# Kernel tuning notes

Measured on AMD Instinct MI355X. Metric: run time of the kernel, lower is better.

The kernel has to match this reference:

```python
import jax, jax.numpy as jnp
import numpy as np

B, N, D = 8, 4096, 256
MLP_DIM = int(2.0 * D * 2)  # mlp_expansion_factor * dim * 2


def setup_inputs() -> dict:
    key = jax.random.key(0)
    ks = jax.random.split(key, 16)
    s = 0.02  # small init for MLP linears (torch Linear default is small-uniform)
    return {
        'h':  jax.random.normal(ks[0], (B, N, D), jnp.float32),
        'x1': jax.random.normal(ks[1], (B, N, D, 3), jnp.float32),  # degree 1, m=3
        'x2': jax.random.normal(ks[2], (B, N, D, 5), jnp.float32),  # degree 2, m=5
        # per-degree projections (torch.randn init, unscaled, per source)
        'proj1': jax.random.normal(ks[3], (D, D), jnp.float32),
        'proj2': jax.random.normal(ks[4], (D, D), jnp.float32),
        'pre1':  jax.random.normal(ks[5], (D, D), jnp.float32),
        'pre2':  jax.random.normal(ks[6], (D, D), jnp.float32),
        # per-degree 2-layer MLPs: Linear(2D, MLP_DIM) -> SiLU -> Linear(MLP_DIM, 2D)
        'w1_0': jax.random.normal(ks[7], (2 * D, MLP_DIM), jnp.float32) * s,
        'b1_0': jnp.zeros((MLP_DIM,), jnp.float32),
        'w2_0': jax.random.normal(ks[8], (MLP_DIM, 2 * D), jnp.float32) * s,
        'b2_0': jnp.zeros((2 * D,), jnp.float32),
        'w1_1': jax.random.normal(ks[9], (2 * D, MLP_DIM), jnp.float32) * s,
        'b1_1': jnp.zeros((MLP_DIM,), jnp.float32),
        'w2_1': jax.random.normal(ks[10], (MLP_DIM, 2 * D), jnp.float32) * s,
        'b2_1': jnp.zeros((2 * D,), jnp.float32),
    }


def _one_degree(h, x, pre, proj, w1, b1, w2, b2):
    # x: (b, n, d, m); project channels for the invariant branch
    pm = jnp.einsum('bndm,de->bnem', x, pre)            # (b, n, d, m)
    inv = jnp.sqrt(jnp.sum(pm * pm, axis=-1))           # L2 norm over m -> (b, n, d)
    mlp_in = jnp.concatenate([h, inv], axis=-1)         # (b, n, 2d)
    hid = jax.nn.silu(mlp_in @ w1 + b1)                 # (b, n, mlp_dim)
    out = hid @ w2 + b2                                 # (b, n, 2d)
    m1, m2 = out[..., :D], out[..., D:]                 # each (b, n, d)
    p = jnp.einsum('bndm,de->bnem', x, proj)            # (b, n, d, m)
    mod = p * m2[..., None]                             # per-channel gating over m
    return m1, mod


def reference(h, x1, x2, proj1, proj2, pre1, pre2,
              w1_0, b1_0, w2_0, b2_0, w1_1, b1_1, w2_1, b2_1):
    m1_a, mod1 = _one_degree(h, x1, pre1, proj1, w1_0, b1_0, w2_0, b2_0)
    m1_b, mod2 = _one_degree(h, x2, pre2, proj2, w1_1, b1_1, w2_1, b2_1)
    h_new = h + m1_a + m1_b
    return (h_new, x1 + mod1, x2 + mod2)
```

## Files before the change

kernel.cpp:

```cpp
#include <hip/hip_runtime.h>
#include <hip/hip_bf16.h>

#define BN    32768
#define DD    256
#define MLPD  1024
#define TWOD  512

typedef __attribute__((ext_vector_type(8))) short short8;
typedef __attribute__((ext_vector_type(4))) float f32x4;

using bf16 = __hip_bfloat16;

__device__ __forceinline__ float bf2f(bf16 v){ return __bfloat162float(v); }
__device__ __forceinline__ bf16  f2bf(float v){ return __float2bfloat16(v); }

__device__ __forceinline__ void gl_lds16(const bf16* g, bf16* l) {
    __builtin_amdgcn_global_load_lds(
        (const __attribute__((address_space(1))) void*)(g),
        (__attribute__((address_space(3))) void*)(l),
        16, 0, 0);
}

__global__ void kprep(const float* __restrict__ pre1, const float* __restrict__ pre2,
                      const float* __restrict__ proj1, const float* __restrict__ proj2,
                      const float* __restrict__ w10, const float* __restrict__ w11,
                      const float* __restrict__ w20, const float* __restrict__ w21,
                      const float* __restrict__ h,
                      bf16* __restrict__ preT, bf16* __restrict__ projT,
                      bf16* __restrict__ w1T, bf16* __restrict__ w2T,
                      bf16* __restrict__ hbf)
{
    const long T0 = 131072, T1 = 131072, T2 = 1048576, T3 = 1048576, T4 = 8388608;
    const long total = T0 + T1 + T2 + T3 + T4;
    for (long i = (long)blockIdx.x * blockDim.x + threadIdx.x; i < total;
         i += (long)gridDim.x * blockDim.x) {
        long t = i;
        if (t < T0) {
            int d = (int)(t >> 16); int r = (int)(t & 65535); int e = r >> 8, k = r & 255;
            preT[t] = f2bf((d ? pre2 : pre1)[k*256 + e]);
        } else if ((t -= T0) < T1) {
            int d = (int)(t >> 16); int r = (int)(t & 65535); int e = r >> 8, k = r & 255;
            projT[t] = f2bf((d ? proj2 : proj1)[k*256 + e]);
        } else if ((t -= T1) < T2) {
            int d = (int)(t >> 19); int r = (int)(t & 524287); int j = r >> 9, k = r & 511;
            w1T[t] = f2bf((d ? w11 : w10)[k*1024 + j]);
        } else if ((t -= T2) < T3) {
            int d = (int)(t >> 19); int r = (int)(t & 524287); int n = r >> 10, k = r & 1023;
            w2T[t] = f2bf((d ? w21 : w20)[k*512 + n]);
        } else {
            t -= T3;
            hbf[t] = f2bf(h[t]);
        }
    }
}

template<int M, int ST>
__global__ __launch_bounds__(256) void kxT(const float* __restrict__ x,
                                           char* __restrict__ outb)
{
    __shared__ float raw[8*256*M];
    const int tid = threadIdx.x;
    const long tok0 = (long)blockIdx.x * 8;
    const float4* src = (const float4*)(x + tok0*256*M);
    const int n4 = (8*256*M)/4;
    for (int i = tid; i < n4; i += 256)
        ((float4*)raw)[i] = src[i];
    __syncthreads();
    const int nOut = 8*M*32;
    for (int i = tid; i < nOut; i += 256) {
        int d8 = i & 31;
        int tm = i >> 5;
        int t = tm / M, m = tm - t*M;
        short8 v;
#pragma unroll
        for (int j = 0; j < 8; j++) {
            bf16 bv = f2bf(raw[(t*256 + d8*8 + j)*M + m]);
            v[j] = *reinterpret_cast<short*>(&bv);
        }
        *(short8*)(outb + (size_t)(tok0 + t)*ST + m*512 + d8*16) = v;
    }
}

template<int M, int ST, bool MOD>
__global__ __launch_bounds__(256) void kxg(const char* __restrict__ xtb,
                                           const bf16* __restrict__ Bmat,
                                           bf16* __restrict__ invp,
                                           const bf16* __restrict__ m2p,
                                           const float* __restrict__ x,
                                           float* __restrict__ xout)
{
    __shared__ bf16 As[M*512];
    __shared__ bf16 Bs[8192];
    const int tid = threadIdx.x;
    const int lane = tid & 63, w = tid >> 6;
    const int lh = lane >> 4, l15 = lane & 15;
    const long tok0 = (long)blockIdx.x * 16;

    f32x4 acc[M][4];
#pragma unroll
    for (int m = 0; m < M; m++)
#pragma unroll
        for (int c = 0; c < 4; c++) acc[m][c] = (f32x4){0.f,0.f,0.f,0.f};

    for (int kc = 0; kc < 8; kc++) {
        for (int m = w; m < M; m += 4) {
            const char* src = xtb + (size_t)(tok0 + (lane >> 2))*ST
                              + m*512 + kc*64 + (lane & 3)*16;
            gl_lds16((const bf16*)src, As + m*512);
        }
#pragma unroll
        for (int i = 0; i < 4; i++) {
            int row = i*64 + (tid >> 2);
            gl_lds16(Bmat + row*256 + kc*32 + (tid & 3)*8, Bs + i*2048 + w*512);
        }
        __syncthreads();
        short8 a[M], b[4];
#pragma unroll
        for (int m = 0; m < M; m++)
            a[m] = *(const short8*)&As[m*512 + l15*32 + lh*8];
#pragma unroll
        for (int ct = 0; ct < 4; ct++)
            b[ct] = *(const short8*)&Bs[(w*64 + ct*16 + l15)*32 + lh*8];
#pragma unroll
        for (int m = 0; m < M; m++)
#pragma unroll
            for (int ct = 0; ct < 4; ct++)
                acc[m][ct] = __builtin_amdgcn_mfma_f32_16x16x32_bf16(a[m], b[ct], acc[m][ct], 0, 0, 0);
        __syncthreads();
    }

    if constexpr (!MOD) {
#pragma unroll
        for (int ct = 0; ct < 4; ct++) {
#pragma unroll
            for (int i = 0; i < 4; i++) {
                long t = tok0 + lh*4 + i;
                int e = w*64 + ct*16 + l15;
                float s = 0.f;
#pragma unroll
                for (int m = 0; m < M; m++) { float p = acc[m][ct][i]; s += p*p; }
                invp[t*256 + e] = f2bf(sqrtf(s));
            }
        }
    } else {
#pragma unroll
        for (int ct = 0; ct < 4; ct++) {
#pragma unroll
            for (int i = 0; i < 4; i++) {
                long t = tok0 + lh*4 + i;
                int e = w*64 + ct*16 + l15;
                float m2v = bf2f(m2p[t*256 + e]);
#pragma unroll
                for (int m = 0; m < M; m++) {
                    long gi = (t*256 + e)*(long)M + m;
                    xout[gi] = x[gi] + acc[m][ct][i]*m2v;
                }
            }
        }
    }
}

__global__ __launch_bounds__(512) void kmlp1(const bf16* __restrict__ hbf,
                                             const bf16* __restrict__ invws,
                                             const bf16* __restrict__ w1T,
                                             const float* __restrict__ b1_0,
                                             const float* __restrict__ b1_1,
                                             char* __restrict__ x1b,
                                             char* __restrict__ x2b,
                                             bf16* __restrict__ hid1b)
{
    __shared__ bf16 As[128*32];
    __shared__ bf16 Bs[256*32];
    const int tid = threadIdx.x;
    const int lane = tid & 63, w = tid >> 6;
    const int wr = w >> 2, wc = w & 3;
    const int lh = lane >> 4, l15 = lane & 15;

    const int bid   = ((blockIdx.x & 7) << 8) | (blockIdx.x >> 3);
    const int d     = bid >> 10;
    const int r     = bid & 1023;
    const int mtile = r >> 2;
    const int ntile = r & 3;
    const long tok0 = (long)mtile * 128;
    const int  j0   = ntile * 256;

    const bf16* Ahb = hbf   + (size_t)tok0 * 256;
    const bf16* Ain = invws + (size_t)d * BN * 256 + (size_t)tok0 * 256;
    const bf16* Bw  = w1T   + (size_t)d * MLPD * TWOD;
    const float* b1 = d ? b1_1 : b1_0;

    const int srow = tid >> 2;
    const int scol = (tid & 3) * 8;

    f32x4 acc[4][4];
#pragma unroll
    for (int ai = 0; ai < 4; ai++)
#pragma unroll
        for (int bj = 0; bj < 4; bj++) acc[ai][bj] = (f32x4){0.f,0.f,0.f,0.f};

    for (int kc = 0; kc < 16; kc++) {
        {
            const bf16* src = (kc < 8)
                ? Ahb + (size_t)srow*256 + kc*32 + scol
                : Ain + (size_t)srow*256 + (kc - 8)*32 + scol;
            gl_lds16(src, As + w*512);
        }
#pragma unroll
        for (int i = 0; i < 2; i++) {
            gl_lds16(Bw + (size_t)(j0 + i*128 + srow)*512 + kc*32 + scol,
                     Bs + i*4096 + w*512);
        }
        __syncthreads();
        short8 a[4], b[4];
#pragma unroll
        for (int ai = 0; ai < 4; ai++)
            a[ai] = *(const short8*)&As[(wr*64 + ai*16 + l15)*32 + lh*8];
#pragma unroll
        for (int bj = 0; bj < 4; bj++)
            b[bj] = *(const short8*)&Bs[(wc*64 + bj*16 + l15)*32 + lh*8];
#pragma unroll
        for (int ai = 0; ai < 4; ai++)
#pragma unroll
            for (int bj = 0; bj < 4; bj++)
                acc[ai][bj] = __builtin_amdgcn_mfma_f32_16x16x32_bf16(a[ai], b[bj], acc[ai][bj], 0, 0, 0);
        __syncthreads();
    }

#pragma unroll
    for (int ai = 0; ai < 4; ai++) {
#pragma unroll
        for (int bj = 0; bj < 4; bj++) {
#pragma unroll
            for (int i = 0; i < 4; i++) {
                long t = tok0 + wr*64 + ai*16 + lh*4 + i;
                int  j = j0 + wc*64 + bj*16 + l15;
                float v = acc[ai][bj][i] + b1[j];
                float s = v / (1.0f + __expf(-v));
                bf16 sb = f2bf(s);
                if (d == 0) {
                    *(bf16*)(x2b + (size_t)t*5120 + 2560 + j*2) = sb;
                } else {
                    if (j < 768) *(bf16*)(x1b + (size_t)t*3072 + 1536 + j*2) = sb;
                    else         hid1b[t*256 + (j - 768)] = sb;
                }
            }
        }
    }
}

__global__ __launch_bounds__(512) void kmlp2(const char* __restrict__ x1b,
                                             const char* __restrict__ x2b,
                                             const bf16* __restrict__ hid1b,
                                             const bf16* __restrict__ w2T,
                                             const float* __restrict__ b2_0,
                                             const float* __restrict__ b2_1,
                                             const float* __restrict__ h,
                                             bf16* __restrict__ m2ws,
                                             float* __restrict__ hout)
{
    __shared__ bf16 As[128*32];
    __shared__ bf16 Bs[256*32];
    const int tid = threadIdx.x;
    const int lane = tid & 63, w = tid >> 6;
    const int wr = w >> 2, wc = w & 3;
    const int lh = lane >> 4, l15 = lane & 15;

    const int bid   = (blockIdx.x & 7)*96 + (blockIdx.x >> 3);
    const int mtile = bid / 3;
    const int slot  = bid - mtile*3;
    const long tok0 = (long)mtile * 128;
    const bool is_m1 = (slot == 0);
    const int n0  = is_m1 ? 0 : 256;
    const int dm2 = is_m1 ? 0 : (slot - 1);
    const int nIter = is_m1 ? 64 : 32;

    const int srow = tid >> 2;
    const int scol = (tid & 3) * 8;

    f32x4 acc[4][4];
#pragma unroll
    for (int ai = 0; ai < 4; ai++)
#pragma unroll
        for (int bj = 0; bj < 4; bj++) acc[ai][bj] = (f32x4){0.f,0.f,0.f,0.f};

    for (int it = 0; it < nIter; it++) {
        const int d  = is_m1 ? (it >> 5) : dm2;
        const int kk = it & 31;
        {
            const bf16* src;
            if (d == 0)
                src = (const bf16*)(x2b + (size_t)(tok0 + srow)*5120 + 2560
                                    + kk*64 + (tid & 3)*16);
            else if (kk < 24)
                src = (const bf16*)(x1b + (size_t)(tok0 + srow)*3072 + 1536
                                    + kk*64 + (tid & 3)*16);
            else
                src = hid1b + (size_t)(tok0 + srow)*256 + (kk - 24)*32 + scol;
            gl_lds16(src, As + w*512);
        }
        const bf16* Bw = w2T + (size_t)d * TWOD * MLPD;
#pragma unroll
        for (int i = 0; i < 2; i++) {
            gl_lds16(Bw + (size_t)(n0 + i*128 + srow)*MLPD + kk*32 + scol,
                     Bs + i*4096 + w*512);
        }
        __syncthreads();
        short8 a[4], b[4];
#pragma unroll
        for (int ai = 0; ai < 4; ai++)
            a[ai] = *(const short8*)&As[(wr*64 + ai*16 + l15)*32 + lh*8];
#pragma unroll
        for (int bj = 0; bj < 4; bj++)
            b[bj] = *(const short8*)&Bs[(wc*64 + bj*16 + l15)*32 + lh*8];
#pragma unroll
        for (int ai = 0; ai < 4; ai++)
#pragma unroll
            for (int bj = 0; bj < 4; bj++)
                acc[ai][bj] = __builtin_amdgcn_mfma_f32_16x16x32_bf16(a[ai], b[bj], acc[ai][bj], 0, 0, 0);
        __syncthreads();
    }

#pragma unroll
    for (int ai = 0; ai < 4; ai++) {
#pragma unroll
        for (int bj = 0; bj < 4; bj++) {
#pragma unroll
            for (int i = 0; i < 4; i++) {
                long t = tok0 + wr*64 + ai*16 + lh*4 + i;
                int  n = n0 + wc*64 + bj*16 + l15;
                float v = acc[ai][bj][i];
                if (is_m1) {
                    v += b2_0[n] + b2_1[n];
                    hout[t*256 + n] = h[t*256 + n] + v;
                } else {
                    v += (dm2 ? b2_1 : b2_0)[n];
                    m2ws[(size_t)dm2 * BN * 256 + t*256 + (n - 256)] = f2bf(v);
                }
            }
        }
    }
}

extern "C" void kernel_launch(void* const* d_in, const int* in_sizes, int n_in,
                              void* d_out, int out_size, void* d_ws, size_t ws_size,
                              hipStream_t stream)
{
    const float* h     = (const float*)d_in[0];
    const float* x1    = (const float*)d_in[1];
    const float* x2    = (const float*)d_in[2];
    const float* proj1 = (const float*)d_in[3];
    const float* proj2 = (const float*)d_in[4];
    const float* pre1  = (const float*)d_in[5];
    const float* pre2  = (const float*)d_in[6];
    const float* w10   = (const float*)d_in[7];
    const float* b10   = (const float*)d_in[8];
    const float* w20   = (const float*)d_in[9];
    const float* b20   = (const float*)d_in[10];
    const float* w11   = (const float*)d_in[11];
    const float* b11   = (const float*)d_in[12];
    const float* w21   = (const float*)d_in[13];
    const float* b21   = (const float*)d_in[14];

    bf16* preT  = (bf16*)d_ws;
    bf16* projT = preT  + 131072;
    bf16* w1T   = projT + 131072;
    bf16* w2T   = w1T   + 1048576;
    bf16* hbf   = w2T   + 1048576;
    bf16* invm2 = hbf   + 8388608;
    bf16* hid1b = invm2 + 16777216;
    if (ws_size < (size_t)35913728 * 2) return;

    float* hout  = (float*)d_out;
    float* x1out = hout + (size_t)8388608;
    float* x2out = hout + (size_t)33554432;
    char* x1b = (char*)x1out;
    char* x2b = (char*)x2out;

    kprep<<<8192, 256, 0, stream>>>(pre1, pre2, proj1, proj2, w10, w11, w20, w21,
                                    h, preT, projT, w1T, w2T, hbf);
    kxT<3, 3072><<<4096, 256, 0, stream>>>(x1, x1b);
    kxT<5, 5120><<<4096, 256, 0, stream>>>(x2, x2b);
    kxg<3, 3072, false><<<2048, 256, 0, stream>>>(x1b, preT, invm2,
                                                  nullptr, nullptr, nullptr);
    kxg<5, 5120, false><<<2048, 256, 0, stream>>>(x2b, preT + 65536,
                                                  invm2 + (size_t)BN*256,
                                                  nullptr, nullptr, nullptr);
    kmlp1<<<2048, 512, 0, stream>>>(hbf, invm2, w1T, b10, b11, x1b, x2b, hid1b);
    kmlp2<<<768, 512, 0, stream>>>(x1b, x2b, hid1b, w2T, b20, b21, h, invm2, hout);
    kxg<3, 3072, true><<<2048, 256, 0, stream>>>(x1b, projT, nullptr,
                                                 invm2, x1, x1out);
    kxg<5, 5120, true><<<2048, 256, 0, stream>>>(x2b, projT + 65536, nullptr,
                                                 invm2 + (size_t)BN*256, x2, x2out);
}
```

Baseline: 670.9 us.

## Fuse x transpose/bf16 conversion with invariant-norm projection GEMM

Merges the kernel that transposes x to bf16 with the kernel that multiplies it by pre and takes the L2 norm. The bf16 tile is now kept in shared memory and fed straight to the MFMA loop, so the transposed buffer is no longer read back from global memory and two launches go away. The trade-off is that the transpose now loads one token at a time with two barriers per token, which adds serialization and more shared memory per block and may lower occupancy.

```diff
diff --git a/kernel.cpp b/kernel.cpp
--- a/kernel.cpp
+++ b/kernel.cpp
@@ -55,36 +55,83 @@
 }
 
 template<int M, int ST>
-__global__ __launch_bounds__(256) void kxT(const float* __restrict__ x,
-                                           char* __restrict__ outb)
-{
-    __shared__ float raw[8*256*M];
+__global__ __launch_bounds__(256) void kxti(const float* __restrict__ x,
+                                            char* __restrict__ outb,
+                                            const bf16* __restrict__ Bmat,
+                                            bf16* __restrict__ invp)
+{
+    __shared__ float raw[256*M];
+    __shared__ bf16  img[M*16*264];
+    __shared__ bf16  Bs[8192];
     const int tid = threadIdx.x;
-    const long tok0 = (long)blockIdx.x * 8;
-    const float4* src = (const float4*)(x + tok0*256*M);
-    const int n4 = (8*256*M)/4;
-    for (int i = tid; i < n4; i += 256)
-        ((float4*)raw)[i] = src[i];
-    __syncthreads();
-    const int nOut = 8*M*32;
-    for (int i = tid; i < nOut; i += 256) {
-        int d8 = i & 31;
-        int tm = i >> 5;
-        int t = tm / M, m = tm - t*M;
-        short8 v;
-#pragma unroll
-        for (int j = 0; j < 8; j++) {
-            bf16 bv = f2bf(raw[(t*256 + d8*8 + j)*M + m]);
-            v[j] = *reinterpret_cast<short*>(&bv);
-        }
-        *(short8*)(outb + (size_t)(tok0 + t)*ST + m*512 + d8*16) = v;
-    }
-}
-
-template<int M, int ST, bool MOD>
+    const int lane = tid & 63, w = tid >> 6;
+    const int lh = lane >> 4, l15 = lane & 15;
+    const long tok0 = (long)blockIdx.x * 16;
+
+    for (int t = 0; t < 16; t++) {
+        const float4* src = (const float4*)(x + (tok0 + t)*256*M);
+        for (int i = tid; i < 64*M; i += 256)
+            ((float4*)raw)[i] = src[i];
+        __syncthreads();
+        if (tid < M*32) {
+            int m = tid >> 5, d8 = tid & 31;
+            short8 v;
+#pragma unroll
+            for (int j = 0; j < 8; j++) {
+                bf16 bv = f2bf(raw[(d8*8 + j)*M + m]);
+                v[j] = *reinterpret_cast<short*>(&bv);
+            }
+            *(short8*)&img[(m*16 + t)*264 + d8*8] = v;
+            *(short8*)(outb + (size_t)(tok0 + t)*ST + m*512 + d8*16) = v;
+        }
+        __syncthreads();
+    }
+
+    f32x4 acc[M][4];
+#pragma unroll
+    for (int m = 0; m < M; m++)
+#pragma unroll
+        for (int c = 0; c < 4; c++) acc[m][c] = (f32x4){0.f,0.f,0.f,0.f};
+
+    for (int kc = 0; kc < 8; kc++) {
+#pragma unroll
+        for (int i = 0; i < 4; i++) {
+            int row = i*64 + (tid >> 2);
+            gl_lds16(Bmat + row*256 + kc*32 + (tid & 3)*8, Bs + i*2048 + w*512);
+        }
+        __syncthreads();
+        short8 a[M], b[4];
+#pragma unroll
+        for (int m = 0; m < M; m++)
+            a[m] = *(const short8*)&img[(m*16 + l15)*264 + kc*32 + lh*8];
+#pragma unroll
+        for (int ct = 0; ct < 4; ct++)
+            b[ct] = *(const short8*)&Bs[(w*64 + ct*16 + l15)*32 + lh*8];
+#pragma unroll
+        for (int m = 0; m < M; m++)
+#pragma unroll
+            for (int ct = 0; ct < 4; ct++)
+                acc[m][ct] = __builtin_amdgcn_mfma_f32_16x16x32_bf16(a[m], b[ct], acc[m][ct], 0, 0, 0);
+        __syncthreads();
+    }
+
+#pragma unroll
+    for (int ct = 0; ct < 4; ct++) {
+#pragma unroll
+        for (int i = 0; i < 4; i++) {
+            long t = tok0 + lh*4 + i;
+            int e = w*64 + ct*16 + l15;
+            float s = 0.f;
+#pragma unroll
+            for (int m = 0; m < M; m++) { float p = acc[m][ct][i]; s += p*p; }
+            invp[t*256 + e] = f2bf(sqrtf(s));
+        }
+    }
+}
+
+template<int M, int ST>
 __global__ __launch_bounds__(256) void kxg(const char* __restrict__ xtb,
                                            const bf16* __restrict__ Bmat,
-                                           bf16* __restrict__ invp,
                                            const bf16* __restrict__ m2p,
                                            const float* __restrict__ x,
                                            float* __restrict__ xout)
@@ -129,32 +176,17 @@
         __syncthreads();
     }
 
-    if constexpr (!MOD) {
-#pragma unroll
-        for (int ct = 0; ct < 4; ct++) {
-#pragma unroll
-            for (int i = 0; i < 4; i++) {
-                long t = tok0 + lh*4 + i;
-                int e = w*64 + ct*16 + l15;
-                float s = 0.f;
-#pragma unroll
-                for (int m = 0; m < M; m++) { float p = acc[m][ct][i]; s += p*p; }
-                invp[t*256 + e] = f2bf(sqrtf(s));
-            }
-        }
-    } else {
-#pragma unroll
-        for (int ct = 0; ct < 4; ct++) {
-#pragma unroll
-            for (int i = 0; i < 4; i++) {
-                long t = tok0 + lh*4 + i;
-                int e = w*64 + ct*16 + l15;
-                float m2v = bf2f(m2p[t*256 + e]);
-#pragma unroll
-                for (int m = 0; m < M; m++) {
-                    long gi = (t*256 + e)*(long)M + m;
-                    xout[gi] = x[gi] + acc[m][ct][i]*m2v;
-                }
+#pragma unroll
+    for (int ct = 0; ct < 4; ct++) {
+#pragma unroll
+        for (int i = 0; i < 4; i++) {
+            long t = tok0 + lh*4 + i;
+            int e = w*64 + ct*16 + l15;
+            float m2v = bf2f(m2p[t*256 + e]);
+#pragma unroll
+            for (int m = 0; m < M; m++) {
+                long gi = (t*256 + e)*(long)M + m;
+                xout[gi] = x[gi] + acc[m][ct][i]*m2v;
             }
         }
     }
@@ -378,17 +410,12 @@
 
     kprep<<<8192, 256, 0, stream>>>(pre1, pre2, proj1, proj2, w10, w11, w20, w21,
                                     h, preT, projT, w1T, w2T, hbf);
-    kxT<3, 3072><<<4096, 256, 0, stream>>>(x1, x1b);
-    kxT<5, 5120><<<4096, 256, 0, stream>>>(x2, x2b);
-    kxg<3, 3072, false><<<2048, 256, 0, stream>>>(x1b, preT, invm2,
-                                                  nullptr, nullptr, nullptr);
-    kxg<5, 5120, false><<<2048, 256, 0, stream>>>(x2b, preT + 65536,
-                                                  invm2 + (size_t)BN*256,
-                                                  nullptr, nullptr, nullptr);
+    kxti<3, 3072><<<2048, 256, 0, stream>>>(x1, x1b, preT, invm2);
+    kxti<5, 5120><<<2048, 256, 0, stream>>>(x2, x2b, preT + 65536,
+                                            invm2 + (size_t)BN*256);
     kmlp1<<<2048, 512, 0, stream>>>(hbf, invm2, w1T, b10, b11, x1b, x2b, hid1b);
     kmlp2<<<768, 512, 0, stream>>>(x1b, x2b, hid1b, w2T, b20, b21, h, invm2, hout);
-    kxg<3, 3072, true><<<2048, 256, 0, stream>>>(x1b, projT, nullptr,
-                                                 invm2, x1, x1out);
-    kxg<5, 5120, true><<<2048, 256, 0, stream>>>(x2b, projT + 65536, nullptr,
-                                                 invm2 + (size_t)BN*256, x2, x2out);
-}
+    kxg<3, 3072><<<2048, 256, 0, stream>>>(x1b, projT, invm2, x1, x1out);
+    kxg<5, 5120><<<2048, 256, 0, stream>>>(x2b, projT + 65536,
+                                           invm2 + (size_t)BN*256, x2, x2out);
+}
```

Result: slower. 694.6 us (+3.5%).
